# Performance work log

Measured on AMD Instinct MI355X. Metric: run time of the kernel, lower is better.

## Reference

```python
import jax, jax.numpy as jnp
import numpy as np
from jax.scipy.linalg import expm

D_LOGIC = 128
D_MEM = 16
SO_DIM = D_MEM * (D_MEM - 1) // 2  # 120


def _linear_init(key, fan_in, shape):
    bound = 1.0 / np.sqrt(fan_in)
    return jax.random.uniform(key, shape, jnp.float32, -bound, bound)


def setup_inputs() -> dict:
    key = jax.random.key(0)
    ks = jax.random.split(key, 14)
    B, S = 4, 128
    return {
        "x_logic": jax.random.normal(ks[0], (B, S, D_LOGIC), jnp.float32),
        "x_memory": jax.random.normal(ks[1], (B, S, D_MEM), jnp.float32),
        # W_Q / W_K
        "Wq": _linear_init(ks[2], D_LOGIC, (D_LOGIC, D_LOGIC)),
        "bq": _linear_init(ks[3], D_LOGIC, (D_LOGIC,)),
        "Wk": _linear_init(ks[4], D_LOGIC, (D_LOGIC, D_LOGIC)),
        "bk": _linear_init(ks[5], D_LOGIC, (D_LOGIC,)),
        # gamma_net: Linear(d_logic, 2*d_logic) -> Tanh -> Linear(2*d_logic, so_dim)
        "W1": _linear_init(ks[6], D_LOGIC, (2 * D_LOGIC, D_LOGIC)),
        "b1": _linear_init(ks[7], D_LOGIC, (2 * D_LOGIC,)),
        "W2": _linear_init(ks[8], 2 * D_LOGIC, (SO_DIM, 2 * D_LOGIC)),
        "b2": _linear_init(ks[9], 2 * D_LOGIC, (SO_DIM,)),
        # out_proj: Linear(d_memory, d_memory)
        "Wo": _linear_init(ks[10], D_MEM, (D_MEM, D_MEM)),
        "bo": _linear_init(ks[11], D_MEM, (D_MEM,)),
    }


def reference(x_logic, x_memory, Wq, bq, Wk, bk, W1, b1, W2, b2, Wo, bo):
    B, S, d_logic = x_logic.shape
    dm = x_memory.shape[-1]

    # attention over logic stream
    Q = x_logic @ Wq.T + bq
    K = x_logic @ Wk.T + bk
    attn = jax.nn.softmax(
        jnp.einsum("bjd,bid->bji", Q, K) / jnp.sqrt(jnp.float32(d_logic)), axis=-1
    )  # [B, S(j), S(i)]

    # per-pair Lie-algebra params: delta[b,j,i] = x_logic[b,j] - x_logic[b,i]
    delta = x_logic[:, :, None, :] - x_logic[:, None, :, :]  # [B,S,S,d_logic]
    h = jnp.tanh(delta @ W1.T + b1)
    lie = h @ W2.T + b2  # [B,S,S,so_dim]

    # scatter into skew-symmetric matrices [B,S,S,dm,dm]
    r, c = np.triu_indices(dm, k=1)
    skew = jnp.zeros((B, S, S, dm, dm), x_logic.dtype)
    skew = skew.at[..., r, c].set(lie)
    skew = skew.at[..., c, r].set(-lie)

    # Lie-group exponential -> orthogonal transport matrices
    T_all = expm(skew)  # [B,S,S,dm,dm]

    # transported[b,j,i,:] = T[b,j,i] @ x_memory[b,i]
    transported = jnp.einsum("bjide,bie->bjid", T_all, x_memory)

    # attention-weighted aggregation over i
    settled = jnp.einsum("bji,bjid->bjd", attn, transported)  # [B,S,dm]

    out = settled @ Wo.T + bo
    return out, T_all
```

## Files before the change

### kernel.cpp

```cpp
#include <hip/hip_runtime.h>
#include <hip/hip_fp16.h>

#define S_LEN 128
#define DLOG  128
#define DMEM  16
#define SO    120
#define HDIM  256

typedef _Float16 v8h __attribute__((ext_vector_type(8)));
typedef __fp16 v2hf __attribute__((ext_vector_type(2)));
typedef float v4f __attribute__((ext_vector_type(4)));

union PkU { v2hf h; unsigned u; };
union V8U { v8h v; int u[4]; };

__device__ __forceinline__ v8h splat8(float x) {
  _Float16 h = (_Float16)x;
  v8h v = {h, h, h, h, h, h, h, h};
  return v;
}

__global__ __launch_bounds__(512) void qku_kernel(
    const float* __restrict__ xl, const float* __restrict__ Wq,
    const float* __restrict__ bq, const float* __restrict__ Wk,
    const float* __restrict__ bk, const float* __restrict__ W1,
    float* __restrict__ Q, float* __restrict__ K, float* __restrict__ u) {
  int bj = blockIdx.x, t = threadIdx.x;
  __shared__ float xs[128];
  if (t < 128) xs[t] = xl[bj * 128 + t];
  __syncthreads();
  const float* wr;
  float acc;
  int o;
  if (t < 128) {
    o = t; wr = Wq + o * 128; acc = bq[o];
  } else if (t < 256) {
    o = t - 128; wr = Wk + o * 128; acc = bk[o];
  } else {
    o = t - 256; wr = W1 + o * 128; acc = 0.f;
  }
  #pragma unroll 4
  for (int d = 0; d < 128; ++d) acc = fmaf(xs[d], wr[d], acc);
  if (t < 128) Q[bj * 128 + o] = acc;
  else if (t < 256) K[bj * 128 + o] = acc;
  else u[bj * 256 + o] = acc;
}

__global__ __launch_bounds__(128) void attn_kernel(
    const float* __restrict__ Q, const float* __restrict__ K,
    float* __restrict__ attn) {
  int bj = blockIdx.x, b = bj >> 7, i = threadIdx.x;
  __shared__ float qs[128];
  __shared__ float red[128];
  qs[i] = Q[bj * 128 + i];
  __syncthreads();
  const float* kr = K + (b * 128 + i) * 128;
  float s = 0.f;
  #pragma unroll 4
  for (int d = 0; d < 128; ++d) s = fmaf(qs[d], kr[d], s);
  s *= 0.08838834764831845f;
  red[i] = s;
  __syncthreads();
  for (int off = 64; off; off >>= 1) {
    if (i < off) red[i] = fmaxf(red[i], red[i + off]);
    __syncthreads();
  }
  float m = red[0];
  __syncthreads();
  float e = expf(s - m);
  red[i] = e;
  __syncthreads();
  for (int off = 64; off; off >>= 1) {
    if (i < off) red[i] += red[i + off];
    __syncthreads();
  }
  attn[(size_t)bj * 128 + i] = e / red[0];
}

__global__ __launch_bounds__(256) void h_from_u_kernel(
    const float* __restrict__ u, const float* __restrict__ b1,
    _Float16* __restrict__ hG, const float* __restrict__ W2g,
    _Float16* __restrict__ w2h) {
  if (blockIdx.x >= 2048) {
    int idx = ((blockIdx.x - 2048) * 256 + threadIdx.x) * 4;
    float4 v = *(const float4*)(W2g + idx);
    PkU u0, u1;
    u0.h = __builtin_amdgcn_cvt_pkrtz(v.x, v.y);
    u1.h = __builtin_amdgcn_cvt_pkrtz(v.z, v.w);
    uint2 pk = {u0.u, u1.u};
    *(uint2*)(w2h + idx) = pk;
    return;
  }
  int tid = blockIdx.x * 256 + threadIdx.x;
  #pragma unroll
  for (int g = 0; g < 4; ++g) {
    int unit = tid + g * 524288;
    int p = unit >> 5;
    int o0 = (unit & 31) * 8;
    int bj = p >> 7;
    int b = bj >> 7;
    int i = p & 127;
    const float* uj = u + bj * 256 + o0;
    const float* ui = u + (size_t)(b * 128 + i) * 256 + o0;
    const float* bb = b1 + o0;
    float4 j0 = *(const float4*)uj, j1 = *(const float4*)(uj + 4);
    float4 i0 = *(const float4*)ui, i1 = *(const float4*)(ui + 4);
    float4 c0 = *(const float4*)bb, c1 = *(const float4*)(bb + 4);
    float xv[8] = {j0.x - i0.x + c0.x, j0.y - i0.y + c0.y,
                   j0.z - i0.z + c0.z, j0.w - i0.w + c0.w,
                   j1.x - i1.x + c1.x, j1.y - i1.y + c1.y,
                   j1.z - i1.z + c1.z, j1.w - i1.w + c1.w};
    float rv[8];
    #pragma unroll
    for (int k = 0; k < 8; ++k) {
      float x = xv[k];
      float ax = fabsf(x);
      float e = __expf(-2.f * ax);
      float r = __fdividef(1.f - e, 1.f + e);
      rv[k] = copysignf(r, x);
    }
    V8U out;
    #pragma unroll
    for (int k = 0; k < 4; ++k) {
      PkU pu;
      pu.h = __builtin_amdgcn_cvt_pkrtz(rv[2 * k], rv[2 * k + 1]);
      out.u[k] = (int)pu.u;
    }
    *(v8h*)(hG + (size_t)p * 512 + o0) = out.v;
  }
}

__global__ __launch_bounds__(512) void lie_kernel(
    const _Float16* __restrict__ w2h, const float* __restrict__ b2g,
    float* __restrict__ Tg) {
  __shared__ _Float16 w2t[128 * 136];
  int t = threadIdx.x, lane = t & 63;
  int wu = __builtin_amdgcn_readfirstlane(t >> 6);
  int pbase = blockIdx.x * 128 + wu * 16;
  int nn = lane & 15, q = lane >> 4;
  const _Float16* hf = (const _Float16*)Tg;

  for (int idx = t; idx < 1088; idx += 512) w2t[16320 + idx] = (_Float16)0.f;

  v4f acc[8];
  #pragma unroll
  for (int tt = 0; tt < 8; ++tt) acc[tt] = (v4f){0.f, 0.f, 0.f, 0.f};

  const _Float16* hrow = hf + (size_t)(pbase + nn) * 512;
  for (int khalf = 0; khalf < 2; ++khalf) {
    __syncthreads();
    for (int idx = t; idx < 1920; idx += 512) {
      int row = idx >> 4, cu = (idx & 15) * 8;
      *(v8h*)(w2t + row * 136 + cu) =
          *(const v8h*)(w2h + row * 256 + khalf * 128 + cu);
    }
    __syncthreads();
    #pragma unroll
    for (int ks = 0; ks < 4; ++ks) {
      v8h ah = *(const v8h*)(hrow + khalf * 128 + ks * 32 + 8 * q);
      #pragma unroll
      for (int tt = 0; tt < 8; ++tt) {
        const v8h bf = *(const v8h*)(w2t + (16 * tt + nn) * 136 + ks * 32 + 8 * q);
        acc[tt] = __builtin_amdgcn_mfma_f32_16x16x32_f16(ah, bf, acc[tt], 0, 0, 0);
      }
    }
  }

  _Float16* hw = (_Float16*)Tg;
  #pragma unroll
  for (int tt = 0; tt < 8; ++tt) {
    int n16 = 16 * tt + nn;
    if (n16 < 120) {
      float bb = b2g[n16];
      float fr_ = floorf((31.0f - sqrtf(961.0f - 8.0f * (float)n16)) * 0.5f);
      int r = (int)fr_;
      int Sr = 15 * r - ((r * (r - 1)) >> 1);
      int c = n16 - Sr + r + 1;
      #pragma unroll
      for (int reg = 0; reg < 4; ++reg) {
        size_t p = (size_t)(pbase + 4 * q + reg);
        _Float16 hv = (_Float16)(acc[tt][reg] + bb);
        _Float16* Ab = hw + p * 512 + 256;
        Ab[r * 16 + c] = hv;
        Ab[c * 16 + r] = -hv;
      }
    }
  }
  #pragma unroll
  for (int reg = 0; reg < 4; ++reg) {
    size_t p = (size_t)(pbase + 4 * q + reg);
    (hw + p * 512 + 256)[nn * 17] = (_Float16)0.f;
  }
}

__device__ __forceinline__ void split8(const float* x, v8h& hi, v8h& lo) {
  union U { v8h v; v2hf p[4]; } H, L;
  #pragma unroll
  for (int i = 0; i < 4; ++i) {
    float a = x[2 * i], b = x[2 * i + 1];
    v2hf h = __builtin_amdgcn_cvt_pkrtz(a, b);
    float ra = (float)h[0], rb = (float)h[1];
    v2hf l = __builtin_amdgcn_cvt_pkrtz(a - ra, b - rb);
    H.p[i] = h;
    L.p[i] = l;
  }
  hi = H.v;
  lo = L.v;
}

__global__ __launch_bounds__(256) void expm_kernel(
    float* __restrict__ Tg, const float* __restrict__ attn,
    const float* __restrict__ xm, float* __restrict__ part) {
  __shared__ char lds[10240] __attribute__((aligned(16)));
  __shared__ float sred[4][16];
  int t = threadIdx.x, lane = t & 63;
  int wu = __builtin_amdgcn_readfirstlane(t >> 6);
  int pbase = blockIdx.x * 8 + wu * 2;
  int nn = lane & 15, q = lane >> 4, b8 = (q & 1) * 8;
  float* ErB = (float*)(lds + wu * 2560);
  const _Float16* hf = (const _Float16*)Tg;

  int idxA = ((2 * (q & 1)) * 16 + nn) * 4;
  int idxB = idxA + 64;

  float scv[2];
  int sv[2];
  V8U Apk[2], BfA[2];
  v4f Af[2];
  #pragma unroll
  for (int j = 0; j < 2; ++j) {
    size_t p = (size_t)(pbase + j);
    const _Float16* Ap = hf + p * 512 + 256;
    v8h rowh = *(const v8h*)(Ap + nn * 16 + b8);
    float s2 = 0.f;
    #pragma unroll
    for (int k = 0; k < 8; ++k) {
      float xf = (float)rowh[k];
      s2 = fmaf(xf, xf, s2);
    }
    #pragma unroll
    for (int off = 1; off < 64; off <<= 1) s2 += __shfl_xor(s2, off, 64);
    float bound = 0.5f * sqrtf(s2);
    int s = 0;
    while (bound > 1.0f && s < 12) { bound *= 0.5f; s++; }
    sv[j] = __builtin_amdgcn_readfirstlane(s);
    scv[j] = ldexpf(1.0f, -s);
    v8h sch = splat8(scv[j]);
    V8U ap;
    ap.v = rowh * sch;
    #pragma unroll
    for (int i = 0; i < 4; ++i) {
      Apk[j].u[i] = ap.u[i];
      BfA[j].u[i] = ap.u[i] ^ 0x80008000;
    }
    #pragma unroll
    for (int reg = 0; reg < 4; ++reg)
      Af[j][reg] = (float)Ap[(4 * q + reg) * 16 + nn] * scv[j];
  }

  V8U IC1, IC2;
  #pragma unroll
  for (int i = 0; i < 4; ++i) {
    float d0 = (b8 + 2 * i == nn) ? 1.f : 0.f;
    float d1 = (b8 + 2 * i + 1 == nn) ? 1.f : 0.f;
    PkU u1, u2;
    u1.h = __builtin_amdgcn_cvt_pkrtz(10.666667f * d0, 10.666667f * d1);
    u2.h = __builtin_amdgcn_cvt_pkrtz(2.1333333f * d0, 2.1333333f * d1);
    IC1.u[i] = (int)u1.u;
    IC2.u[i] = (int)u2.u;
  }

  v4f z4 = {0.f, 0.f, 0.f, 0.f};

  v4f cB[2];
  #pragma unroll
  for (int j = 0; j < 2; ++j)
    cB[j] = __builtin_amdgcn_mfma_f32_16x16x32_f16(Apk[j].v, BfA[j].v, z4, 0, 0, 0);

  V8U fB[2];
  #pragma unroll
  for (int j = 0; j < 2; ++j) {
    PkU u0, u1;
    u0.h = __builtin_amdgcn_cvt_pkrtz(cB[j][0], cB[j][1]);
    u1.h = __builtin_amdgcn_cvt_pkrtz(cB[j][2], cB[j][3]);
    fB[j].u[0] = __builtin_amdgcn_ds_bpermute(idxA, (int)u0.u);
    fB[j].u[1] = __builtin_amdgcn_ds_bpermute(idxA, (int)u1.u);
    fB[j].u[2] = __builtin_amdgcn_ds_bpermute(idxB, (int)u0.u);
    fB[j].u[3] = __builtin_amdgcn_ds_bpermute(idxB, (int)u1.u);
  }

  v4f cB2[2];
  #pragma unroll
  for (int j = 0; j < 2; ++j)
    cB2[j] = __builtin_amdgcn_mfma_f32_16x16x32_f16(fB[j].v, fB[j].v, z4, 0, 0, 0);

  V8U fB2[2];
  #pragma unroll
  for (int j = 0; j < 2; ++j) {
    PkU u0, u1;
    u0.h = __builtin_amdgcn_cvt_pkrtz(cB2[j][0], cB2[j][1]);
    u1.h = __builtin_amdgcn_cvt_pkrtz(cB2[j][2], cB2[j][3]);
    fB2[j].u[0] = __builtin_amdgcn_ds_bpermute(idxA, (int)u0.u);
    fB2[j].u[1] = __builtin_amdgcn_ds_bpermute(idxA, (int)u1.u);
    fB2[j].u[2] = __builtin_amdgcn_ds_bpermute(idxB, (int)u0.u);
    fB2[j].u[3] = __builtin_amdgcn_ds_bpermute(idxB, (int)u1.u);
  }

  v8h k1a = splat8(7.9365079e-4f);
  v8h k1b = splat8(0.17777778f);
  v8h k2a = splat8(8.8183422e-5f);
  v8h k2b = splat8(2.5396825e-2f);
  V8U M1[2], M2[2];
  #pragma unroll
  for (int j = 0; j < 2; ++j) {
    M1[j].v = fB2[j].v * k1a + (fB[j].v * k1b + IC1.v);
    M2[j].v = fB2[j].v * k2a + (fB[j].v * k2b + IC2.v);
  }

  v4f Cc[2], Qc[2];
  #pragma unroll
  for (int j = 0; j < 2; ++j) {
    v4f c3m = __builtin_amdgcn_mfma_f32_16x16x32_f16(M1[j].v, fB2[j].v, z4, 0, 0, 0);
    v4f c4m = __builtin_amdgcn_mfma_f32_16x16x32_f16(M2[j].v, fB2[j].v, z4, 0, 0, 0);
    #pragma unroll
    for (int reg = 0; reg < 4; ++reg) {
      float dg = (4 * q + reg == nn) ? 1.f : 0.f;
      Cc[j][reg] = fmaf(c3m[reg], 2.44140625e-4f,
                        fmaf(cB[j][reg], 0.25f, dg + Af[j][reg]));
      Qc[j][reg] = fmaf(c4m[reg], 2.44140625e-4f, cB[j][reg] * 0.083333333f);
    }
  }

  V8U fQ[2];
  #pragma unroll
  for (int j = 0; j < 2; ++j) {
    PkU u0, u1;
    u0.h = __builtin_amdgcn_cvt_pkrtz(Qc[j][0], Qc[j][1]);
    u1.h = __builtin_amdgcn_cvt_pkrtz(Qc[j][2], Qc[j][3]);
    fQ[j].u[0] = __builtin_amdgcn_ds_bpermute(idxA, (int)u0.u);
    fQ[j].u[1] = __builtin_amdgcn_ds_bpermute(idxA, (int)u1.u);
    fQ[j].u[2] = __builtin_amdgcn_ds_bpermute(idxB, (int)u0.u);
    fQ[j].u[3] = __builtin_amdgcn_ds_bpermute(idxB, (int)u1.u);
  }

  v4f E[2];
  #pragma unroll
  for (int j = 0; j < 2; ++j) {
    v4f c5 = __builtin_amdgcn_mfma_f32_16x16x32_f16(Apk[j].v, fQ[j].v, z4, 0, 0, 0);
    E[j] = Cc[j] + c5 * 0.5f;
  }

  int smax = max(sv[0], sv[1]);
  for (int it = 0; it < smax; ++it) {
    #pragma unroll
    for (int j = 0; j < 2; ++j) {
      if (it < sv[j]) {
        float* Erp = ErB + j * 320;
        PkU u0, u1;
        u0.h = __builtin_amdgcn_cvt_pkrtz(E[j][0], E[j][1]);
        u1.h = __builtin_amdgcn_cvt_pkrtz(E[j][2], E[j][3]);
        V8U bfe;
        bfe.u[0] = __builtin_amdgcn_ds_bpermute(idxA, (int)u0.u);
        bfe.u[1] = __builtin_amdgcn_ds_bpermute(idxA, (int)u1.u);
        bfe.u[2] = __builtin_amdgcn_ds_bpermute(idxB, (int)u0.u);
        bfe.u[3] = __builtin_amdgcn_ds_bpermute(idxB, (int)u1.u);
        #pragma unroll
        for (int reg = 0; reg < 4; ++reg)
          Erp[(4 * q + reg) * 20 + nn] = E[j][reg];
        asm volatile("s_waitcnt lgkmcnt(0)" ::: "memory");
        float4 a0 = *(const float4*)(Erp + nn * 20 + b8);
        float4 a1 = *(const float4*)(Erp + nn * 20 + b8 + 4);
        float xa[8] = {a0.x, a0.y, a0.z, a0.w, a1.x, a1.y, a1.z, a1.w};
        v8h ahi, alo;
        split8(xa, ahi, alo);
        v8h Ecat = (q < 2) ? ahi : alo;
        v4f z = {0.f, 0.f, 0.f, 0.f};
        E[j] = __builtin_amdgcn_mfma_f32_16x16x32_f16(Ecat, bfe.v, z, 0, 0, 0);
      }
    }
  }

  float pacc[4] = {0.f, 0.f, 0.f, 0.f};
  #pragma unroll
  for (int j = 0; j < 2; ++j) {
    int p = pbase + j;
    float* dst = Tg + (size_t)p * 256;
    #pragma unroll
    for (int reg = 0; reg < 4; ++reg)
      dst[(4 * q + reg) * 16 + nn] = E[j][reg];
    int b = p >> 14, i = p & 127;
    float xv = xm[((b << 7) + i) * 16 + nn];
    float aw = attn[(size_t)p] * xv;
    #pragma unroll
    for (int reg = 0; reg < 4; ++reg)
      pacc[reg] = fmaf(aw, E[j][reg], pacc[reg]);
  }
  #pragma unroll
  for (int reg = 0; reg < 4; ++reg) {
    #pragma unroll
    for (int off = 1; off < 16; off <<= 1)
      pacc[reg] += __shfl_xor(pacc[reg], off, 64);
  }
  if (nn == 0) {
    #pragma unroll
    for (int reg = 0; reg < 4; ++reg) sred[wu][4 * q + reg] = pacc[reg];
  }
  __syncthreads();
  if (t < 16)
    part[(size_t)blockIdx.x * 16 + t] =
        sred[0][t] + sred[1][t] + sred[2][t] + sred[3][t];
}

__global__ __launch_bounds__(64) void settle_fin_kernel(
    const float* __restrict__ part, const float* __restrict__ Wo,
    const float* __restrict__ bo, float* __restrict__ outp) {
  int bj = blockIdx.x, t = threadIdx.x;
  int r = t & 15, e0 = t >> 4;
  const float* pb = part + (size_t)bj * 256;
  float s = pb[e0 * 16 + r] + pb[(e0 + 4) * 16 + r] +
            pb[(e0 + 8) * 16 + r] + pb[(e0 + 12) * 16 + r];
  __shared__ float sf[64];
  sf[t] = s;
  __syncthreads();
  if (t < 16) sf[t] = sf[t] + sf[16 + t] + sf[32 + t] + sf[48 + t];
  __syncthreads();
  if (t < 16) {
    float o = bo[t];
    const float* wr = Wo + t * 16;
    #pragma unroll
    for (int c = 0; c < 16; ++c) o = fmaf(wr[c], sf[c], o);
    outp[bj * 16 + t] = o;
  }
}

extern "C" void kernel_launch(void* const* d_in, const int* in_sizes, int n_in,
                              void* d_out, int out_size, void* d_ws,
                              size_t ws_size, hipStream_t stream) {
  const float* xl = (const float*)d_in[0];
  const float* xm = (const float*)d_in[1];
  const float* Wq = (const float*)d_in[2];
  const float* bq = (const float*)d_in[3];
  const float* Wk = (const float*)d_in[4];
  const float* bk = (const float*)d_in[5];
  const float* W1 = (const float*)d_in[6];
  const float* b1 = (const float*)d_in[7];
  const float* W2 = (const float*)d_in[8];
  const float* b2 = (const float*)d_in[9];
  const float* Wo = (const float*)d_in[10];
  const float* bo = (const float*)d_in[11];
  float* outp = (float*)d_out;
  float* Tg = outp + 8192;
  float* wsf = (float*)d_ws;
  float* Q = wsf;
  float* K = wsf + 65536;
  float* attn = wsf + 131072;
  _Float16* w2h = (_Float16*)Q;
  float* u = wsf + 196608;
  float* part = wsf + 196608;

  hipLaunchKernelGGL(qku_kernel, dim3(512), dim3(512), 0, stream, xl, Wq, bq, Wk, bk, W1, Q, K, u);
  hipLaunchKernelGGL(attn_kernel, dim3(512), dim3(128), 0, stream, Q, K, attn);
  hipLaunchKernelGGL(h_from_u_kernel, dim3(2078), dim3(256), 0, stream, u, b1, (_Float16*)Tg, W2, w2h);
  hipLaunchKernelGGL(lie_kernel, dim3(512), dim3(512), 0, stream, w2h, b2, Tg);
  hipLaunchKernelGGL(expm_kernel, dim3(8192), dim3(256), 0, stream, Tg, attn, xm, part);
  hipLaunchKernelGGL(settle_fin_kernel, dim3(512), dim3(64), 0, stream, part, Wo, bo, outp);
}
```

Measured before the change: 214.9 us.

## Coalesce QK/attn matvec loads and stage skew scatter through LDS

```diff
diff --git a/kernel.cpp b/kernel.cpp
--- a/kernel.cpp
+++ b/kernel.cpp
@@ -26,39 +26,56 @@
     const float* __restrict__ bk, const float* __restrict__ W1,
     float* __restrict__ Q, float* __restrict__ K, float* __restrict__ u) {
   int bj = blockIdx.x, t = threadIdx.x;
-  __shared__ float xs[128];
-  if (t < 128) xs[t] = xl[bj * 128 + t];
-  __syncthreads();
-  const float* wr;
-  float acc;
-  int o;
-  if (t < 128) {
-    o = t; wr = Wq + o * 128; acc = bq[o];
-  } else if (t < 256) {
-    o = t - 128; wr = Wk + o * 128; acc = bk[o];
-  } else {
-    o = t - 256; wr = W1 + o * 128; acc = 0.f;
-  }
+  int lane = t & 63, wu = t >> 6;
+  int half = lane >> 5, l5 = lane & 31;
+  float4 xv = *(const float4*)(xl + bj * 128 + 4 * l5);
+  int seg = wu >> 1;
+  const float* wb;
+  if (seg == 0) wb = Wq;
+  else if (seg == 1) wb = Wk - 128 * 128;
+  else wb = W1 - 256 * 128;
   #pragma unroll 4
-  for (int d = 0; d < 128; ++d) acc = fmaf(xs[d], wr[d], acc);
-  if (t < 128) Q[bj * 128 + o] = acc;
-  else if (t < 256) K[bj * 128 + o] = acc;
-  else u[bj * 256 + o] = acc;
+  for (int step = 0; step < 32; ++step) {
+    int ro = wu * 64 + 2 * step + half;
+    float4 wv = *(const float4*)(wb + ro * 128 + 4 * l5);
+    float v = fmaf(wv.x, xv.x, fmaf(wv.y, xv.y, fmaf(wv.z, xv.z, wv.w * xv.w)));
+    v += __shfl_xor(v, 1, 64);
+    v += __shfl_xor(v, 2, 64);
+    v += __shfl_xor(v, 4, 64);
+    v += __shfl_xor(v, 8, 64);
+    v += __shfl_xor(v, 16, 64);
+    if (l5 == 0) {
+      if (seg == 0) Q[bj * 128 + ro] = v + bq[ro];
+      else if (seg == 1) K[bj * 128 + (ro - 128)] = v + bk[ro - 128];
+      else u[bj * 256 + (ro - 256)] = v;
+    }
+  }
 }
 
 __global__ __launch_bounds__(128) void attn_kernel(
     const float* __restrict__ Q, const float* __restrict__ K,
     float* __restrict__ attn) {
-  int bj = blockIdx.x, b = bj >> 7, i = threadIdx.x;
-  __shared__ float qs[128];
+  int bj = blockIdx.x, b = bj >> 7, t = threadIdx.x;
+  int lane = t & 63, wu = t >> 6;
+  int half = lane >> 5, l5 = lane & 31;
+  __shared__ float sc[128];
   __shared__ float red[128];
-  qs[i] = Q[bj * 128 + i];
-  __syncthreads();
-  const float* kr = K + (b * 128 + i) * 128;
-  float s = 0.f;
+  float4 qv = *(const float4*)(Q + bj * 128 + 4 * l5);
   #pragma unroll 4
-  for (int d = 0; d < 128; ++d) s = fmaf(qs[d], kr[d], s);
-  s *= 0.08838834764831845f;
+  for (int step = 0; step < 32; ++step) {
+    int ro = wu * 64 + 2 * step + half;
+    float4 kv = *(const float4*)(K + (size_t)(b * 128 + ro) * 128 + 4 * l5);
+    float v = fmaf(kv.x, qv.x, fmaf(kv.y, qv.y, fmaf(kv.z, qv.z, kv.w * qv.w)));
+    v += __shfl_xor(v, 1, 64);
+    v += __shfl_xor(v, 2, 64);
+    v += __shfl_xor(v, 4, 64);
+    v += __shfl_xor(v, 8, 64);
+    v += __shfl_xor(v, 16, 64);
+    if (l5 == 0) sc[ro] = v * 0.08838834764831845f;
+  }
+  __syncthreads();
+  int i = t;
+  float s = sc[i];
   red[i] = s;
   __syncthreads();
   for (int off = 64; off; off >>= 1) {
@@ -166,30 +183,50 @@
     }
   }
 
-  _Float16* hw = (_Float16*)Tg;
+  int rc0[8], rc1[8];
+  float bbv[8];
+  bool val[8];
   #pragma unroll
   for (int tt = 0; tt < 8; ++tt) {
     int n16 = 16 * tt + nn;
-    if (n16 < 120) {
-      float bb = b2g[n16];
-      float fr_ = floorf((31.0f - sqrtf(961.0f - 8.0f * (float)n16)) * 0.5f);
-      int r = (int)fr_;
-      int Sr = 15 * r - ((r * (r - 1)) >> 1);
-      int c = n16 - Sr + r + 1;
-      #pragma unroll
-      for (int reg = 0; reg < 4; ++reg) {
-        size_t p = (size_t)(pbase + 4 * q + reg);
-        _Float16 hv = (_Float16)(acc[tt][reg] + bb);
-        _Float16* Ab = hw + p * 512 + 256;
-        Ab[r * 16 + c] = hv;
-        Ab[c * 16 + r] = -hv;
+    val[tt] = (n16 < 120);
+    float fr_ = floorf((31.0f - sqrtf(961.0f - 8.0f * (float)n16)) * 0.5f);
+    int r = (int)fr_;
+    int Sr = 15 * r - ((r * (r - 1)) >> 1);
+    int c = n16 - Sr + r + 1;
+    rc0[tt] = r * 16 + c;
+    rc1[tt] = c * 16 + r;
+    bbv[tt] = val[tt] ? b2g[n16] : 0.f;
+  }
+
+  _Float16* hw = (_Float16*)Tg;
+  _Float16* aSt = w2t;
+  for (int pass = 0; pass < 2; ++pass) {
+    __syncthreads();
+    #pragma unroll
+    for (int reg = 0; reg < 4; ++reg) {
+      int pidx = 4 * q + reg;
+      if ((pidx >> 3) == pass) {
+        _Float16* ab = aSt + (wu * 8 + (pidx & 7)) * 256;
+        #pragma unroll
+        for (int tt = 0; tt < 8; ++tt) {
+          if (val[tt]) {
+            _Float16 hv = (_Float16)(acc[tt][reg] + bbv[tt]);
+            ab[rc0[tt]] = hv;
+            ab[rc1[tt]] = -hv;
+          }
+        }
+        ab[nn * 17] = (_Float16)0.f;
       }
     }
-  }
-  #pragma unroll
-  for (int reg = 0; reg < 4; ++reg) {
-    size_t p = (size_t)(pbase + 4 * q + reg);
-    (hw + p * 512 + 256)[nn * 17] = (_Float16)0.f;
+    __syncthreads();
+    #pragma unroll
+    for (int k = 0; k < 4; ++k) {
+      int unit = t + k * 512;
+      int lp = unit >> 5, off = (unit & 31) * 8;
+      int g = blockIdx.x * 128 + (lp >> 3) * 16 + pass * 8 + (lp & 7);
+      *(v8h*)(hw + (size_t)g * 512 + 256 + off) = *(const v8h*)(aSt + lp * 256 + off);
+    }
   }
 }
 
```

Result: faster. 201.6 us (-6.2%).
